# Optimization experiments

Hardware: AMD Instinct MI355X
Metric: run time of the kernel (lower is better)

Reference implementation:

```python
import jax, jax.numpy as jnp
import numpy as np

NUM_BINS = 10
HIST_RANGE = 10.0
LN_EPS = 1e-5
NUM_SERVERS = 64
START_IDX = 2 + 2 + NUM_SERVERS  # = 68


def layer_norm(x, g, b):
    mu = jnp.mean(x, axis=-1, keepdims=True)
    var = jnp.mean(jnp.square(x - mu), axis=-1, keepdims=True)
    return (x - mu) * jax.lax.rsqrt(var + LN_EPS) * g + b


def batched_histogram(w):
    # w: [B, S]; replicates np.histogram(w_i, bins=10, range=(0,10)) per row,
    # then normalizes by (sum + 1e-8). Values outside [0,10] are excluded;
    # value == 10 falls in the last bin.
    idx = jnp.clip(jnp.floor(w * (NUM_BINS / HIST_RANGE)).astype(jnp.int32), 0, NUM_BINS - 1)
    mask = ((w >= 0.0) & (w <= HIST_RANGE)).astype(w.dtype)
    oh = jax.nn.one_hot(idx, NUM_BINS, dtype=w.dtype) * mask[..., None]  # [B,S,NB]
    hist = jnp.sum(oh, axis=1)  # [B,NB]
    return hist / (jnp.sum(hist, axis=-1, keepdims=True) + 1e-8)


def setup_inputs() -> dict:
    key = jax.random.key(0)
    ks = jax.random.split(key, 16)
    B, OBS, ACT, H, NB = 65536, 512, 64, 128, NUM_BINS
    COMB = (OBS - NUM_SERVERS) + 128 + 64  # 640

    def lin(k, fin, fout):
        bound = 1.0 / np.sqrt(fin)
        kw, kb = jax.random.split(k)
        return (jax.random.uniform(kw, (fin, fout), jnp.float32, -bound, bound),
                jax.random.uniform(kb, (fout,), jnp.float32, -bound, bound))

    obs = jax.random.uniform(ks[0], (B, OBS), jnp.float32, 0.0, 10.0)
    preference = jax.random.uniform(ks[1], (B, 2), jnp.float32)
    h_w1, h_b1 = lin(ks[2], NB, H)
    h_w2, h_b2 = lin(ks[3], H, H)
    p_w, p_b = lin(ks[4], 2, 64)
    s_w1, s_b1 = lin(ks[5], COMB, 256)
    s_w2, s_b2 = lin(ks[6], 256, 256)
    qd_w, qd_b = lin(ks[7], 256, ACT)
    qe_w, qe_b = lin(ks[8], 256, ACT)
    return {
        'obs': obs, 'preference': preference,
        'h_w1': h_w1, 'h_b1': h_b1,
        'h_ln1_g': jnp.ones((H,)), 'h_ln1_b': jnp.zeros((H,)),
        'h_w2': h_w2, 'h_b2': h_b2,
        'h_ln2_g': jnp.ones((H,)), 'h_ln2_b': jnp.zeros((H,)),
        'p_w': p_w, 'p_b': p_b,
        'p_ln_g': jnp.ones((64,)), 'p_ln_b': jnp.zeros((64,)),
        's_w1': s_w1, 's_b1': s_b1,
        's_ln1_g': jnp.ones((256,)), 's_ln1_b': jnp.zeros((256,)),
        's_w2': s_w2, 's_b2': s_b2,
        's_ln2_g': jnp.ones((256,)), 's_ln2_b': jnp.zeros((256,)),
        'qd_w': qd_w, 'qd_b': qd_b, 'qe_w': qe_w, 'qe_b': qe_b,
    }


def reference(obs, preference,
              h_w1, h_b1, h_ln1_g, h_ln1_b, h_w2, h_b2, h_ln2_g, h_ln2_b,
              p_w, p_b, p_ln_g, p_ln_b,
              s_w1, s_b1, s_ln1_g, s_ln1_b, s_w2, s_b2, s_ln2_g, s_ln2_b,
              qd_w, qd_b, qe_w, qe_b):
    server_workloads = obs[:, START_IDX:START_IDX + NUM_SERVERS]
    obs_wo = jnp.concatenate([obs[:, :START_IDX], obs[:, START_IDX + NUM_SERVERS:]], axis=-1)

    hist = batched_histogram(server_workloads)  # [B, 10]
    h = layer_norm(jax.nn.relu(hist @ h_w1 + h_b1), h_ln1_g, h_ln1_b)
    h = layer_norm(jax.nn.relu(h @ h_w2 + h_b2), h_ln2_g, h_ln2_b)  # [B,128]

    p = layer_norm(jax.nn.relu(preference @ p_w + p_b), p_ln_g, p_ln_b)  # [B,64]

    combined = jnp.concatenate([obs_wo, h, p], axis=-1)  # [B,640]
    s = layer_norm(jax.nn.relu(combined @ s_w1 + s_b1), s_ln1_g, s_ln1_b)
    s = layer_norm(jax.nn.relu(s @ s_w2 + s_b2), s_ln2_g, s_ln2_b)  # [B,256]

    q_delay = s @ qd_w + qd_b   # [B,A]
    q_energy = s @ qe_w + qe_b  # [B,A]
    return jnp.stack([q_delay, q_energy], axis=-1)  # [B,A,2]
```

## Files before the change

### kernel.cpp

```cpp
#include <hip/hip_runtime.h>

typedef __bf16 bf16x8 __attribute__((ext_vector_type(8)));
typedef float  f32x4  __attribute__((ext_vector_type(4)));

#define OFF_W1  0
#define OFF_W2  163840
#define OFF_WQ  229376
#define OFF_WH1 262144
#define OFF_WH2 266240
#define WS_ELEMS 282624

__global__ __launch_bounds__(256) void prep_kernel(
    const float* __restrict__ s_w1, const float* __restrict__ s_w2,
    const float* __restrict__ qd_w, const float* __restrict__ qe_w,
    const float* __restrict__ h_w1, const float* __restrict__ h_w2,
    __bf16* __restrict__ wsb)
{
  int idx = blockIdx.x * 256 + threadIdx.x;
  if (idx >= WS_ELEMS) return;
  float val = 0.f;
  if (idx < OFF_W2) {
    int t = idx;
    int j = t & 7, l = (t >> 3) & 63, rest = t >> 9;
    int nt = rest & 15, ks = rest >> 4;
    int k = ks * 32 + (l >> 4) * 8 + j, n = nt * 16 + (l & 15);
    val = s_w1[k * 256 + n];
  } else if (idx < OFF_WQ) {
    int t = idx - OFF_W2;
    int j = t & 7, l = (t >> 3) & 63, rest = t >> 9;
    int nt = rest & 15, ks = rest >> 4;
    int k = ks * 32 + (l >> 4) * 8 + j, n = nt * 16 + (l & 15);
    val = s_w2[k * 256 + n];
  } else if (idx < OFF_WH1) {
    int t = idx - OFF_WQ;
    int j = t & 7, l = (t >> 3) & 63, rest = t >> 9;
    int nt = rest & 7, ks = rest >> 3;
    int k = ks * 32 + (l >> 4) * 8 + j, n = nt * 16 + (l & 15);
    int a = n >> 1;
    val = (n & 1) ? qe_w[k * 64 + a] : qd_w[k * 64 + a];
  } else if (idx < OFF_WH2) {
    int t = idx - OFF_WH1;
    int j = t & 7, l = (t >> 3) & 63, rest = t >> 9;
    int nt = rest & 7;
    int k = (l >> 4) * 8 + j, n = nt * 16 + (l & 15);
    val = (k < 10) ? h_w1[k * 128 + n] : 0.f;
  } else {
    int t = idx - OFF_WH2;
    int j = t & 7, l = (t >> 3) & 63, rest = t >> 9;
    int nt = rest & 7, ks = rest >> 3;
    int k = ks * 32 + (l >> 4) * 8 + j, n = nt * 16 + (l & 15);
    val = h_w2[k * 128 + n];
  }
  wsb[idx] = (__bf16)val;
}

template<int KSTEPS, int NT_TOT, int NTW>
__device__ __forceinline__ void run_gemm(const __bf16* A, int astride,
    const bf16x8* __restrict__ Bsw, int wave, int lane, f32x4 acc[2][NTW])
{
  const int quad = lane >> 4, ln = lane & 15;
  const int ntb = wave * NTW;
  bf16x8 bcur[NTW];
#pragma unroll
  for (int i = 0; i < NTW; ++i) bcur[i] = Bsw[(ntb + i) * 64 + lane];
#pragma unroll
  for (int ks = 0; ks < KSTEPS; ++ks) {
    bf16x8 bnxt[NTW];
    if (ks + 1 < KSTEPS) {
#pragma unroll
      for (int i = 0; i < NTW; ++i)
        bnxt[i] = Bsw[((ks + 1) * NT_TOT + ntb + i) * 64 + lane];
    }
    bf16x8 a[2];
#pragma unroll
    for (int mt = 0; mt < 2; ++mt)
      a[mt] = *(const bf16x8*)(A + (mt * 16 + ln) * astride + ks * 32 + quad * 8);
#pragma unroll
    for (int mt = 0; mt < 2; ++mt)
#pragma unroll
      for (int i = 0; i < NTW; ++i)
        acc[mt][i] = __builtin_amdgcn_mfma_f32_16x16x32_bf16(a[mt], bcur[i], acc[mt][i], 0, 0, 0);
    if (ks + 1 < KSTEPS) {
#pragma unroll
      for (int i = 0; i < NTW; ++i) bcur[i] = bnxt[i];
    }
  }
}

template<int W, int NTW>
__device__ __forceinline__ void epilogue_ln(f32x4 acc[2][NTW],
    const float* __restrict__ bias, const float* __restrict__ g, const float* __restrict__ bb,
    __bf16* Adst, int dstride, int dstcol0,
    float* red_s, float* red_q, int wave, int lane)
{
  const int quad = lane >> 4, ln = lane & 15;
  float x[2][NTW][4];
#pragma unroll
  for (int i = 0; i < NTW; ++i) {
    int n = (wave * NTW + i) * 16 + ln;
    float b = bias[n];
#pragma unroll
    for (int mt = 0; mt < 2; ++mt)
#pragma unroll
      for (int r = 0; r < 4; ++r)
        x[mt][i][r] = fmaxf(acc[mt][i][r] + b, 0.f);
  }
#pragma unroll
  for (int mt = 0; mt < 2; ++mt) {
    float s[4] = {0, 0, 0, 0}, q[4] = {0, 0, 0, 0};
#pragma unroll
    for (int i = 0; i < NTW; ++i)
#pragma unroll
      for (int r = 0; r < 4; ++r) { s[r] += x[mt][i][r]; q[r] += x[mt][i][r] * x[mt][i][r]; }
#pragma unroll
    for (int m2 = 1; m2 < 16; m2 <<= 1)
#pragma unroll
      for (int r = 0; r < 4; ++r) {
        s[r] += __shfl_xor(s[r], m2, 64);
        q[r] += __shfl_xor(q[r], m2, 64);
      }
    if (ln == 0) {
#pragma unroll
      for (int r = 0; r < 4; ++r) {
        int m = mt * 16 + quad * 4 + r;
        red_s[wave * 32 + m] = s[r];
        red_q[wave * 32 + m] = q[r];
      }
    }
  }
  __syncthreads();
#pragma unroll
  for (int mt = 0; mt < 2; ++mt)
#pragma unroll
    for (int r = 0; r < 4; ++r) {
      int m = mt * 16 + quad * 4 + r;
      float tot = 0.f, totq = 0.f;
#pragma unroll
      for (int w2 = 0; w2 < 8; ++w2) { tot += red_s[w2 * 32 + m]; totq += red_q[w2 * 32 + m]; }
      float mu = tot / (float)W;
      float var = totq / (float)W - mu * mu;
      float rs = rsqrtf(var + 1e-5f);
#pragma unroll
      for (int i = 0; i < NTW; ++i) {
        int n = (wave * NTW + i) * 16 + ln;
        float o = (x[mt][i][r] - mu) * rs * g[n] + bb[n];
        Adst[m * dstride + dstcol0 + n] = (__bf16)o;
      }
    }
  __syncthreads();
}

__global__ __launch_bounds__(512, 4) void critic_kernel(
    const float* __restrict__ obs, const float* __restrict__ pref,
    const float* __restrict__ h_b1, const float* __restrict__ h_g1, const float* __restrict__ h_bb1,
    const float* __restrict__ h_b2, const float* __restrict__ h_g2, const float* __restrict__ h_bb2,
    const float* __restrict__ p_w, const float* __restrict__ p_b,
    const float* __restrict__ p_g, const float* __restrict__ p_bb,
    const float* __restrict__ s_b1, const float* __restrict__ s_g1, const float* __restrict__ s_bb1,
    const float* __restrict__ s_b2, const float* __restrict__ s_g2, const float* __restrict__ s_bb2,
    const float* __restrict__ qd_b, const float* __restrict__ qe_b,
    const __bf16* __restrict__ wsb, float* __restrict__ out)
{
  __shared__ __align__(16) __bf16 A_comb[32 * 648];
  __shared__ __align__(16) __bf16 A_s[32 * 264];
  __shared__ __align__(16) __bf16 A_h[32 * 40];
  __shared__ float red_s[256];
  __shared__ float red_q[256];

  const int tid = threadIdx.x;
  const int wave = tid >> 6, lane = tid & 63;
  const int rowbase = blockIdx.x * 32;

  float pw0 = p_w[lane], pw1 = p_w[64 + lane], pb = p_b[lane];
  float pg = p_g[lane], pbb = p_bb[lane];
#pragma unroll
  for (int r = 0; r < 4; ++r) {
    int row = wave * 4 + r;
    int grow = rowbase + row;
    const float* orow = obs + (size_t)grow * 512;
#pragma unroll
    for (int j = 0; j < 7; ++j) {
      int col = lane + 64 * j;
      int src = (col < 68) ? col : col + 64;
      A_comb[row * 648 + col] = (__bf16)orow[src];
    }
    float w = orow[68 + lane];
    int bi = (int)floorf(w);
    bi = bi < 0 ? 0 : (bi > 9 ? 9 : bi);
    bool valid = (w >= 0.f) && (w <= 10.f);
    float tot = 0.f, mine = 0.f;
#pragma unroll
    for (int b = 0; b < 10; ++b) {
      unsigned long long mk = __ballot(valid && (bi == b));
      float c = (float)__popcll(mk);
      tot += c;
      if (lane == b) mine = c;
    }
    float inv = 1.f / (tot + 1e-8f);
    if (lane < 32) A_h[row * 40 + lane] = (__bf16)((lane < 10) ? mine * inv : 0.f);
    float a0 = pref[grow * 2], a1 = pref[grow * 2 + 1];
    float v = fmaxf(fmaf(a0, pw0, fmaf(a1, pw1, pb)), 0.f);
    float s1 = v, s2 = v * v;
#pragma unroll
    for (int m2 = 1; m2 < 64; m2 <<= 1) {
      s1 += __shfl_xor(s1, m2, 64);
      s2 += __shfl_xor(s2, m2, 64);
    }
    float mu = s1 * (1.f / 64.f);
    float var = s2 * (1.f / 64.f) - mu * mu;
    float o = (v - mu) * rsqrtf(var + 1e-5f) * pg + pbb;
    A_comb[row * 648 + 576 + lane] = (__bf16)o;
  }
  __syncthreads();

  {
    f32x4 acc[2][1] = {};
    run_gemm<1, 8, 1>(A_h, 40, (const bf16x8*)(wsb + OFF_WH1), wave, lane, acc);
    epilogue_ln<128, 1>(acc, h_b1, h_g1, h_bb1, A_s, 264, 0, red_s, red_q, wave, lane);
  }
  {
    f32x4 acc[2][1] = {};
    run_gemm<4, 8, 1>(A_s, 264, (const bf16x8*)(wsb + OFF_WH2), wave, lane, acc);
    epilogue_ln<128, 1>(acc, h_b2, h_g2, h_bb2, A_comb, 648, 448, red_s, red_q, wave, lane);
  }
  {
    f32x4 acc[2][2] = {};
    run_gemm<20, 16, 2>(A_comb, 648, (const bf16x8*)(wsb + OFF_W1), wave, lane, acc);
    epilogue_ln<256, 2>(acc, s_b1, s_g1, s_bb1, A_s, 264, 0, red_s, red_q, wave, lane);
  }
  {
    f32x4 acc[2][2] = {};
    run_gemm<8, 16, 2>(A_s, 264, (const bf16x8*)(wsb + OFF_W2), wave, lane, acc);
    epilogue_ln<256, 2>(acc, s_b2, s_g2, s_bb2, A_s, 264, 0, red_s, red_q, wave, lane);
  }
  {
    f32x4 acc[2][1] = {};
    run_gemm<8, 8, 1>(A_s, 264, (const bf16x8*)(wsb + OFF_WQ), wave, lane, acc);
    const int quad = lane >> 4, ln = lane & 15;
    int n = wave * 16 + ln;
    float qb = (n & 1) ? qe_b[n >> 1] : qd_b[n >> 1];
#pragma unroll
    for (int mt = 0; mt < 2; ++mt)
#pragma unroll
      for (int r = 0; r < 4; ++r) {
        int m = mt * 16 + quad * 4 + r;
        out[(size_t)(rowbase + m) * 128 + n] = acc[mt][0][r] + qb;
      }
  }
}

extern "C" void kernel_launch(void* const* d_in, const int* in_sizes, int n_in,
                              void* d_out, int out_size, void* d_ws, size_t ws_size,
                              hipStream_t stream) {
  const float* obs    = (const float*)d_in[0];
  const float* pref   = (const float*)d_in[1];
  const float* h_w1   = (const float*)d_in[2];
  const float* h_b1   = (const float*)d_in[3];
  const float* h_g1   = (const float*)d_in[4];
  const float* h_bb1  = (const float*)d_in[5];
  const float* h_w2   = (const float*)d_in[6];
  const float* h_b2   = (const float*)d_in[7];
  const float* h_g2   = (const float*)d_in[8];
  const float* h_bb2  = (const float*)d_in[9];
  const float* p_w    = (const float*)d_in[10];
  const float* p_b    = (const float*)d_in[11];
  const float* p_g    = (const float*)d_in[12];
  const float* p_bb   = (const float*)d_in[13];
  const float* s_w1   = (const float*)d_in[14];
  const float* s_b1   = (const float*)d_in[15];
  const float* s_g1   = (const float*)d_in[16];
  const float* s_bb1  = (const float*)d_in[17];
  const float* s_w2   = (const float*)d_in[18];
  const float* s_b2   = (const float*)d_in[19];
  const float* s_g2   = (const float*)d_in[20];
  const float* s_bb2  = (const float*)d_in[21];
  const float* qd_w   = (const float*)d_in[22];
  const float* qd_b   = (const float*)d_in[23];
  const float* qe_w   = (const float*)d_in[24];
  const float* qe_b   = (const float*)d_in[25];

  __bf16* wsb = (__bf16*)d_ws;
  int B = in_sizes[0] / 512;
  int nblocks = B / 32;

  prep_kernel<<<(WS_ELEMS + 255) / 256, 256, 0, stream>>>(s_w1, s_w2, qd_w, qe_w, h_w1, h_w2, wsb);
  critic_kernel<<<nblocks, 512, 0, stream>>>(
      obs, pref, h_b1, h_g1, h_bb1, h_b2, h_g2, h_bb2,
      p_w, p_b, p_g, p_bb, s_b1, s_g1, s_bb1, s_b2, s_g2, s_bb2,
      qd_b, qe_b, (const __bf16*)wsb, (float*)d_out);
}
```

Baseline: 377.5 us.

## Halve rows per block to 16, raise occupancy, vectorize obs loads

Each block now handles 16 batch rows instead of 32, so each wave issues one MFMA row tile per step. The launch bound rises to 8 blocks per CU and shared memory is cut, which raises occupancy and the block count. The obs gather now uses float4 loads with bf16x4 stores, and the layernorm reduction scratch is packed into float2. The cost is that each weight fragment loaded from global or L2 is reused across half as many rows, roughly doubling weight traffic per output row.

```diff
diff --git a/kernel.cpp b/kernel.cpp
--- a/kernel.cpp
+++ b/kernel.cpp
@@ -1,6 +1,7 @@
 #include <hip/hip_runtime.h>
 
 typedef __bf16 bf16x8 __attribute__((ext_vector_type(8)));
+typedef __bf16 bf16x4 __attribute__((ext_vector_type(4)));
 typedef float  f32x4  __attribute__((ext_vector_type(4)));
 
 #define OFF_W1  0
@@ -56,7 +57,7 @@
 
 template<int KSTEPS, int NT_TOT, int NTW>
 __device__ __forceinline__ void run_gemm(const __bf16* A, int astride,
-    const bf16x8* __restrict__ Bsw, int wave, int lane, f32x4 acc[2][NTW])
+    const bf16x8* __restrict__ Bsw, int wave, int lane, f32x4 acc[NTW])
 {
   const int quad = lane >> 4, ln = lane & 15;
   const int ntb = wave * NTW;
@@ -71,15 +72,10 @@
       for (int i = 0; i < NTW; ++i)
         bnxt[i] = Bsw[((ks + 1) * NT_TOT + ntb + i) * 64 + lane];
     }
-    bf16x8 a[2];
-#pragma unroll
-    for (int mt = 0; mt < 2; ++mt)
-      a[mt] = *(const bf16x8*)(A + (mt * 16 + ln) * astride + ks * 32 + quad * 8);
-#pragma unroll
-    for (int mt = 0; mt < 2; ++mt)
-#pragma unroll
-      for (int i = 0; i < NTW; ++i)
-        acc[mt][i] = __builtin_amdgcn_mfma_f32_16x16x32_bf16(a[mt], bcur[i], acc[mt][i], 0, 0, 0);
+    bf16x8 a = *(const bf16x8*)(A + ln * astride + ks * 32 + quad * 8);
+#pragma unroll
+    for (int i = 0; i < NTW; ++i)
+      acc[i] = __builtin_amdgcn_mfma_f32_16x16x32_bf16(a, bcur[i], acc[i], 0, 0, 0);
     if (ks + 1 < KSTEPS) {
 #pragma unroll
       for (int i = 0; i < NTW; ++i) bcur[i] = bnxt[i];
@@ -88,69 +84,62 @@
 }
 
 template<int W, int NTW>
-__device__ __forceinline__ void epilogue_ln(f32x4 acc[2][NTW],
+__device__ __forceinline__ void epilogue_ln(f32x4 acc[NTW],
     const float* __restrict__ bias, const float* __restrict__ g, const float* __restrict__ bb,
     __bf16* Adst, int dstride, int dstcol0,
-    float* red_s, float* red_q, int wave, int lane)
+    float2* red, int wave, int lane)
 {
   const int quad = lane >> 4, ln = lane & 15;
-  float x[2][NTW][4];
+  float x[NTW][4];
 #pragma unroll
   for (int i = 0; i < NTW; ++i) {
     int n = (wave * NTW + i) * 16 + ln;
     float b = bias[n];
 #pragma unroll
-    for (int mt = 0; mt < 2; ++mt)
-#pragma unroll
-      for (int r = 0; r < 4; ++r)
-        x[mt][i][r] = fmaxf(acc[mt][i][r] + b, 0.f);
-  }
-#pragma unroll
-  for (int mt = 0; mt < 2; ++mt) {
-    float s[4] = {0, 0, 0, 0}, q[4] = {0, 0, 0, 0};
-#pragma unroll
-    for (int i = 0; i < NTW; ++i)
-#pragma unroll
-      for (int r = 0; r < 4; ++r) { s[r] += x[mt][i][r]; q[r] += x[mt][i][r] * x[mt][i][r]; }
-#pragma unroll
-    for (int m2 = 1; m2 < 16; m2 <<= 1)
-#pragma unroll
-      for (int r = 0; r < 4; ++r) {
-        s[r] += __shfl_xor(s[r], m2, 64);
-        q[r] += __shfl_xor(q[r], m2, 64);
-      }
-    if (ln == 0) {
-#pragma unroll
-      for (int r = 0; r < 4; ++r) {
-        int m = mt * 16 + quad * 4 + r;
-        red_s[wave * 32 + m] = s[r];
-        red_q[wave * 32 + m] = q[r];
-      }
-    }
+    for (int r = 0; r < 4; ++r)
+      x[i][r] = fmaxf(acc[i][r] + b, 0.f);
+  }
+  float s[4] = {0, 0, 0, 0}, q[4] = {0, 0, 0, 0};
+#pragma unroll
+  for (int i = 0; i < NTW; ++i)
+#pragma unroll
+    for (int r = 0; r < 4; ++r) { s[r] += x[i][r]; q[r] += x[i][r] * x[i][r]; }
+#pragma unroll
+  for (int m2 = 1; m2 < 16; m2 <<= 1)
+#pragma unroll
+    for (int r = 0; r < 4; ++r) {
+      s[r] += __shfl_xor(s[r], m2, 64);
+      q[r] += __shfl_xor(q[r], m2, 64);
+    }
+  if (ln == 0) {
+#pragma unroll
+    for (int r = 0; r < 4; ++r)
+      red[wave * 16 + quad * 4 + r] = make_float2(s[r], q[r]);
   }
   __syncthreads();
 #pragma unroll
-  for (int mt = 0; mt < 2; ++mt)
-#pragma unroll
-    for (int r = 0; r < 4; ++r) {
-      int m = mt * 16 + quad * 4 + r;
-      float tot = 0.f, totq = 0.f;
-#pragma unroll
-      for (int w2 = 0; w2 < 8; ++w2) { tot += red_s[w2 * 32 + m]; totq += red_q[w2 * 32 + m]; }
-      float mu = tot / (float)W;
-      float var = totq / (float)W - mu * mu;
-      float rs = rsqrtf(var + 1e-5f);
-#pragma unroll
-      for (int i = 0; i < NTW; ++i) {
-        int n = (wave * NTW + i) * 16 + ln;
-        float o = (x[mt][i][r] - mu) * rs * g[n] + bb[n];
-        Adst[m * dstride + dstcol0 + n] = (__bf16)o;
-      }
-    }
+  for (int r = 0; r < 4; ++r) {
+    int m = quad * 4 + r;
+    float tot = 0.f, totq = 0.f;
+#pragma unroll
+    for (int w2 = 0; w2 < 8; ++w2) {
+      float2 t = red[w2 * 16 + m];
+      tot += t.x; totq += t.y;
+    }
+    float mu = tot / (float)W;
+    float var = totq / (float)W - mu * mu;
+    float rs = rsqrtf(var + 1e-5f);
+#pragma unroll
+    for (int i = 0; i < NTW; ++i) {
+      int n = (wave * NTW + i) * 16 + ln;
+      float o = (x[i][r] - mu) * rs * g[n] + bb[n];
+      Adst[m * dstride + dstcol0 + n] = (__bf16)o;
+    }
+  }
   __syncthreads();
 }
 
-__global__ __launch_bounds__(512, 4) void critic_kernel(
+__global__ __launch_bounds__(512, 8) void critic_kernel(
     const float* __restrict__ obs, const float* __restrict__ pref,
     const float* __restrict__ h_b1, const float* __restrict__ h_g1, const float* __restrict__ h_bb1,
     const float* __restrict__ h_b2, const float* __restrict__ h_g2, const float* __restrict__ h_bb2,
@@ -161,28 +150,32 @@
     const float* __restrict__ qd_b, const float* __restrict__ qe_b,
     const __bf16* __restrict__ wsb, float* __restrict__ out)
 {
-  __shared__ __align__(16) __bf16 A_comb[32 * 648];
-  __shared__ __align__(16) __bf16 A_s[32 * 264];
-  __shared__ __align__(16) __bf16 A_h[32 * 40];
-  __shared__ float red_s[256];
-  __shared__ float red_q[256];
+  __shared__ __align__(16) __bf16 A_comb[16 * 648];
+  __shared__ __align__(16) __bf16 A_s[16 * 264];
+  __shared__ __align__(16) __bf16 A_h[16 * 40];
+  __shared__ float2 red[128];
 
   const int tid = threadIdx.x;
   const int wave = tid >> 6, lane = tid & 63;
-  const int rowbase = blockIdx.x * 32;
+  const int rowbase = blockIdx.x * 16;
 
   float pw0 = p_w[lane], pw1 = p_w[64 + lane], pb = p_b[lane];
   float pg = p_g[lane], pbb = p_bb[lane];
 #pragma unroll
-  for (int r = 0; r < 4; ++r) {
-    int row = wave * 4 + r;
+  for (int r = 0; r < 2; ++r) {
+    int row = wave * 2 + r;
     int grow = rowbase + row;
     const float* orow = obs + (size_t)grow * 512;
 #pragma unroll
-    for (int j = 0; j < 7; ++j) {
-      int col = lane + 64 * j;
-      int src = (col < 68) ? col : col + 64;
-      A_comb[row * 648 + col] = (__bf16)orow[src];
+    for (int j = 0; j < 2; ++j) {
+      int l = lane + 64 * j;
+      if (l < 112) {
+        int src4 = (l < 17) ? l : l + 16;
+        float4 v = *(const float4*)(orow + 4 * src4);
+        bf16x4 o;
+        o[0] = (__bf16)v.x; o[1] = (__bf16)v.y; o[2] = (__bf16)v.z; o[3] = (__bf16)v.w;
+        *(bf16x4*)(&A_comb[row * 648 + 4 * l]) = o;
+      }
     }
     float w = orow[68 + lane];
     int bi = (int)floorf(w);
@@ -214,38 +207,36 @@
   __syncthreads();
 
   {
-    f32x4 acc[2][1] = {};
+    f32x4 acc[1] = {};
     run_gemm<1, 8, 1>(A_h, 40, (const bf16x8*)(wsb + OFF_WH1), wave, lane, acc);
-    epilogue_ln<128, 1>(acc, h_b1, h_g1, h_bb1, A_s, 264, 0, red_s, red_q, wave, lane);
-  }
-  {
-    f32x4 acc[2][1] = {};
+    epilogue_ln<128, 1>(acc, h_b1, h_g1, h_bb1, A_s, 264, 0, red, wave, lane);
+  }
+  {
+    f32x4 acc[1] = {};
     run_gemm<4, 8, 1>(A_s, 264, (const bf16x8*)(wsb + OFF_WH2), wave, lane, acc);
-    epilogue_ln<128, 1>(acc, h_b2, h_g2, h_bb2, A_comb, 648, 448, red_s, red_q, wave, lane);
-  }
-  {
-    f32x4 acc[2][2] = {};
+    epilogue_ln<128, 1>(acc, h_b2, h_g2, h_bb2, A_comb, 648, 448, red, wave, lane);
+  }
+  {
+    f32x4 acc[2] = {};
     run_gemm<20, 16, 2>(A_comb, 648, (const bf16x8*)(wsb + OFF_W1), wave, lane, acc);
-    epilogue_ln<256, 2>(acc, s_b1, s_g1, s_bb1, A_s, 264, 0, red_s, red_q, wave, lane);
-  }
-  {
-    f32x4 acc[2][2] = {};
+    epilogue_ln<256, 2>(acc, s_b1, s_g1, s_bb1, A_s, 264, 0, red, wave, lane);
+  }
+  {
+    f32x4 acc[2] = {};
     run_gemm<8, 16, 2>(A_s, 264, (const bf16x8*)(wsb + OFF_W2), wave, lane, acc);
-    epilogue_ln<256, 2>(acc, s_b2, s_g2, s_bb2, A_s, 264, 0, red_s, red_q, wave, lane);
-  }
-  {
-    f32x4 acc[2][1] = {};
+    epilogue_ln<256, 2>(acc, s_b2, s_g2, s_bb2, A_s, 264, 0, red, wave, lane);
+  }
+  {
+    f32x4 acc[1] = {};
     run_gemm<8, 8, 1>(A_s, 264, (const bf16x8*)(wsb + OFF_WQ), wave, lane, acc);
     const int quad = lane >> 4, ln = lane & 15;
     int n = wave * 16 + ln;
     float qb = (n & 1) ? qe_b[n >> 1] : qd_b[n >> 1];
 #pragma unroll
-    for (int mt = 0; mt < 2; ++mt)
-#pragma unroll
-      for (int r = 0; r < 4; ++r) {
-        int m = mt * 16 + quad * 4 + r;
-        out[(size_t)(rowbase + m) * 128 + n] = acc[mt][0][r] + qb;
-      }
+    for (int r = 0; r < 4; ++r) {
+      int m = quad * 4 + r;
+      out[(size_t)(rowbase + m) * 128 + n] = acc[0][r] + qb;
+    }
   }
 }
 
@@ -281,7 +272,7 @@
 
   __bf16* wsb = (__bf16*)d_ws;
   int B = in_sizes[0] / 512;
-  int nblocks = B / 32;
+  int nblocks = B / 16;
 
   prep_kernel<<<(WS_ELEMS + 255) / 256, 256, 0, stream>>>(s_w1, s_w2, qd_w, qe_w, h_w1, h_w2, wsb);
   critic_kernel<<<nblocks, 512, 0, stream>>>(
```

After: 368.9 us. -2.3%, faster.

## Stream obs A-fragments from global into MFMA, shrink LDS, raise occupancy

Applied to the files above, without the earlier changes.

Stops staging the 448 non-server obs columns in a large LDS buffer. The first big GEMM now loads those A fragments straight from global memory as float4 and converts them to bf16 in registers, using a special offset for the k-step that skips the server columns. Only the hist and pref features stay in a small LDS buffer. This cuts LDS use per block, and launch bounds are raised to 8 blocks per CU. The LN reduction is also packed into float2. The trade-off is uncoalesced, strided global reads inside the MFMA loop with exposed latency, in place of a coalesced prefetch.

```diff
diff --git a/kernel.cpp b/kernel.cpp
--- a/kernel.cpp
+++ b/kernel.cpp
@@ -1,6 +1,7 @@
 #include <hip/hip_runtime.h>
 
 typedef __bf16 bf16x8 __attribute__((ext_vector_type(8)));
+typedef __bf16 bf16x4 __attribute__((ext_vector_type(4)));
 typedef float  f32x4  __attribute__((ext_vector_type(4)));
 
 #define OFF_W1  0
@@ -55,31 +56,29 @@
 }
 
 template<int KSTEPS, int NT_TOT, int NTW>
-__device__ __forceinline__ void run_gemm(const __bf16* A, int astride,
-    const bf16x8* __restrict__ Bsw, int wave, int lane, f32x4 acc[2][NTW])
+__device__ __forceinline__ void run_gemm2(const __bf16* A, int astride,
+    const bf16x8* __restrict__ Bsw, int nt0, int lane, f32x4 acc[2][NTW])
 {
   const int quad = lane >> 4, ln = lane & 15;
-  const int ntb = wave * NTW;
+  const __bf16* ar = A + ln * astride + quad * 8;
   bf16x8 bcur[NTW];
 #pragma unroll
-  for (int i = 0; i < NTW; ++i) bcur[i] = Bsw[(ntb + i) * 64 + lane];
+  for (int i = 0; i < NTW; ++i) bcur[i] = Bsw[(nt0 + i) * 64 + lane];
 #pragma unroll
   for (int ks = 0; ks < KSTEPS; ++ks) {
     bf16x8 bnxt[NTW];
     if (ks + 1 < KSTEPS) {
 #pragma unroll
       for (int i = 0; i < NTW; ++i)
-        bnxt[i] = Bsw[((ks + 1) * NT_TOT + ntb + i) * 64 + lane];
-    }
-    bf16x8 a[2];
-#pragma unroll
-    for (int mt = 0; mt < 2; ++mt)
-      a[mt] = *(const bf16x8*)(A + (mt * 16 + ln) * astride + ks * 32 + quad * 8);
-#pragma unroll
-    for (int mt = 0; mt < 2; ++mt)
-#pragma unroll
-      for (int i = 0; i < NTW; ++i)
-        acc[mt][i] = __builtin_amdgcn_mfma_f32_16x16x32_bf16(a[mt], bcur[i], acc[mt][i], 0, 0, 0);
+        bnxt[i] = Bsw[((ks + 1) * NT_TOT + nt0 + i) * 64 + lane];
+    }
+    bf16x8 a0 = *(const bf16x8*)(ar + ks * 32);
+    bf16x8 a1 = *(const bf16x8*)(ar + 16 * astride + ks * 32);
+#pragma unroll
+    for (int i = 0; i < NTW; ++i) {
+      acc[0][i] = __builtin_amdgcn_mfma_f32_16x16x32_bf16(a0, bcur[i], acc[0][i], 0, 0, 0);
+      acc[1][i] = __builtin_amdgcn_mfma_f32_16x16x32_bf16(a1, bcur[i], acc[1][i], 0, 0, 0);
+    }
     if (ks + 1 < KSTEPS) {
 #pragma unroll
       for (int i = 0; i < NTW; ++i) bcur[i] = bnxt[i];
@@ -88,16 +87,16 @@
 }
 
 template<int W, int NTW>
-__device__ __forceinline__ void epilogue_ln(f32x4 acc[2][NTW],
+__device__ __forceinline__ void epilogue_ln2(f32x4 acc[2][NTW],
     const float* __restrict__ bias, const float* __restrict__ g, const float* __restrict__ bb,
-    __bf16* Adst, int dstride, int dstcol0,
-    float* red_s, float* red_q, int wave, int lane)
+    int nt0, __bf16* Adst, int dstride, int dstcol0,
+    float2* red, int wave, int lane)
 {
   const int quad = lane >> 4, ln = lane & 15;
   float x[2][NTW][4];
 #pragma unroll
   for (int i = 0; i < NTW; ++i) {
-    int n = (wave * NTW + i) * 16 + ln;
+    int n = (nt0 + i) * 16 + ln;
     float b = bias[n];
 #pragma unroll
     for (int mt = 0; mt < 2; ++mt)
@@ -121,11 +120,8 @@
       }
     if (ln == 0) {
 #pragma unroll
-      for (int r = 0; r < 4; ++r) {
-        int m = mt * 16 + quad * 4 + r;
-        red_s[wave * 32 + m] = s[r];
-        red_q[wave * 32 + m] = q[r];
-      }
+      for (int r = 0; r < 4; ++r)
+        red[wave * 32 + mt * 16 + quad * 4 + r] = make_float2(s[r], q[r]);
     }
   }
   __syncthreads();
@@ -136,13 +132,16 @@
       int m = mt * 16 + quad * 4 + r;
       float tot = 0.f, totq = 0.f;
 #pragma unroll
-      for (int w2 = 0; w2 < 8; ++w2) { tot += red_s[w2 * 32 + m]; totq += red_q[w2 * 32 + m]; }
+      for (int w2 = 0; w2 < 8; ++w2) {
+        float2 t = red[w2 * 32 + m];
+        tot += t.x; totq += t.y;
+      }
       float mu = tot / (float)W;
       float var = totq / (float)W - mu * mu;
       float rs = rsqrtf(var + 1e-5f);
 #pragma unroll
       for (int i = 0; i < NTW; ++i) {
-        int n = (wave * NTW + i) * 16 + ln;
+        int n = (nt0 + i) * 16 + ln;
         float o = (x[mt][i][r] - mu) * rs * g[n] + bb[n];
         Adst[m * dstride + dstcol0 + n] = (__bf16)o;
       }
@@ -150,7 +149,7 @@
   __syncthreads();
 }
 
-__global__ __launch_bounds__(512, 4) void critic_kernel(
+__global__ __launch_bounds__(512, 8) void critic_kernel(
     const float* __restrict__ obs, const float* __restrict__ pref,
     const float* __restrict__ h_b1, const float* __restrict__ h_g1, const float* __restrict__ h_bb1,
     const float* __restrict__ h_b2, const float* __restrict__ h_g2, const float* __restrict__ h_bb2,
@@ -161,14 +160,14 @@
     const float* __restrict__ qd_b, const float* __restrict__ qe_b,
     const __bf16* __restrict__ wsb, float* __restrict__ out)
 {
-  __shared__ __align__(16) __bf16 A_comb[32 * 648];
   __shared__ __align__(16) __bf16 A_s[32 * 264];
+  __shared__ __align__(16) __bf16 A2[32 * 200];
   __shared__ __align__(16) __bf16 A_h[32 * 40];
-  __shared__ float red_s[256];
-  __shared__ float red_q[256];
+  __shared__ __align__(16) float2 red[8 * 32];
 
   const int tid = threadIdx.x;
   const int wave = tid >> 6, lane = tid & 63;
+  const int ln = lane & 15, quad = lane >> 4;
   const int rowbase = blockIdx.x * 32;
 
   float pw0 = p_w[lane], pw1 = p_w[64 + lane], pb = p_b[lane];
@@ -178,12 +177,6 @@
     int row = wave * 4 + r;
     int grow = rowbase + row;
     const float* orow = obs + (size_t)grow * 512;
-#pragma unroll
-    for (int j = 0; j < 7; ++j) {
-      int col = lane + 64 * j;
-      int src = (col < 68) ? col : col + 64;
-      A_comb[row * 648 + col] = (__bf16)orow[src];
-    }
     float w = orow[68 + lane];
     int bi = (int)floorf(w);
     bi = bi < 0 ? 0 : (bi > 9 ? 9 : bi);
@@ -200,43 +193,80 @@
     if (lane < 32) A_h[row * 40 + lane] = (__bf16)((lane < 10) ? mine * inv : 0.f);
     float a0 = pref[grow * 2], a1 = pref[grow * 2 + 1];
     float v = fmaxf(fmaf(a0, pw0, fmaf(a1, pw1, pb)), 0.f);
-    float s1 = v, s2 = v * v;
+    float s1v = v, s2v = v * v;
 #pragma unroll
     for (int m2 = 1; m2 < 64; m2 <<= 1) {
-      s1 += __shfl_xor(s1, m2, 64);
-      s2 += __shfl_xor(s2, m2, 64);
-    }
-    float mu = s1 * (1.f / 64.f);
-    float var = s2 * (1.f / 64.f) - mu * mu;
+      s1v += __shfl_xor(s1v, m2, 64);
+      s2v += __shfl_xor(s2v, m2, 64);
+    }
+    float mu = s1v * (1.f / 64.f);
+    float var = s2v * (1.f / 64.f) - mu * mu;
     float o = (v - mu) * rsqrtf(var + 1e-5f) * pg + pbb;
-    A_comb[row * 648 + 576 + lane] = (__bf16)o;
+    A2[row * 200 + 128 + lane] = (__bf16)o;
   }
   __syncthreads();
 
   {
     f32x4 acc[2][1] = {};
-    run_gemm<1, 8, 1>(A_h, 40, (const bf16x8*)(wsb + OFF_WH1), wave, lane, acc);
-    epilogue_ln<128, 1>(acc, h_b1, h_g1, h_bb1, A_s, 264, 0, red_s, red_q, wave, lane);
+    run_gemm2<1, 8, 1>(A_h, 40, (const bf16x8*)(wsb + OFF_WH1), wave, lane, acc);
+    epilogue_ln2<128, 1>(acc, h_b1, h_g1, h_bb1, wave, A_s, 264, 0, red, wave, lane);
   }
   {
     f32x4 acc[2][1] = {};
-    run_gemm<4, 8, 1>(A_s, 264, (const bf16x8*)(wsb + OFF_WH2), wave, lane, acc);
-    epilogue_ln<128, 1>(acc, h_b2, h_g2, h_bb2, A_comb, 648, 448, red_s, red_q, wave, lane);
+    run_gemm2<4, 8, 1>(A_s, 264, (const bf16x8*)(wsb + OFF_WH2), wave, lane, acc);
+    epilogue_ln2<128, 1>(acc, h_b2, h_g2, h_bb2, wave, A2, 200, 0, red, wave, lane);
   }
   {
     f32x4 acc[2][2] = {};
-    run_gemm<20, 16, 2>(A_comb, 648, (const bf16x8*)(wsb + OFF_W1), wave, lane, acc);
-    epilogue_ln<256, 2>(acc, s_b1, s_g1, s_bb1, A_s, 264, 0, red_s, red_q, wave, lane);
+    const bf16x8* B1 = (const bf16x8*)(wsb + OFF_W1);
+    const int nt0 = wave * 2;
+    bf16x8 bcur[2];
+    bcur[0] = B1[nt0 * 64 + lane];
+    bcur[1] = B1[(nt0 + 1) * 64 + lane];
+    const float* ga0 = obs + (size_t)(rowbase + ln) * 512 + quad * 8;
+    const float* ga1 = ga0 + 16 * 512;
+    const __bf16* la = A2 + ln * 200 + quad * 8;
+#pragma unroll
+    for (int ks = 0; ks < 20; ++ks) {
+      bf16x8 bnxt[2];
+      if (ks + 1 < 20) {
+        bnxt[0] = B1[((ks + 1) * 16 + nt0) * 64 + lane];
+        bnxt[1] = B1[((ks + 1) * 16 + nt0 + 1) * 64 + lane];
+      }
+      bf16x8 a0, a1;
+      if (ks < 14) {
+        int o1, o2;
+        if (ks < 2)        { o1 = ks * 32;              o2 = o1 + 4; }
+        else if (ks == 2)  { o1 = (quad == 0) ? 64 : 128; o2 = 132; }
+        else               { o1 = ks * 32 + 64;         o2 = o1 + 4; }
+        float4 v00 = *(const float4*)(ga0 + o1);
+        float4 v01 = *(const float4*)(ga0 + o2);
+        float4 v10 = *(const float4*)(ga1 + o1);
+        float4 v11 = *(const float4*)(ga1 + o2);
+        a0[0] = (__bf16)v00.x; a0[1] = (__bf16)v00.y; a0[2] = (__bf16)v00.z; a0[3] = (__bf16)v00.w;
+        a0[4] = (__bf16)v01.x; a0[5] = (__bf16)v01.y; a0[6] = (__bf16)v01.z; a0[7] = (__bf16)v01.w;
+        a1[0] = (__bf16)v10.x; a1[1] = (__bf16)v10.y; a1[2] = (__bf16)v10.z; a1[3] = (__bf16)v10.w;
+        a1[4] = (__bf16)v11.x; a1[5] = (__bf16)v11.y; a1[6] = (__bf16)v11.z; a1[7] = (__bf16)v11.w;
+      } else {
+        a0 = *(const bf16x8*)(la + (ks - 14) * 32);
+        a1 = *(const bf16x8*)(la + 16 * 200 + (ks - 14) * 32);
+      }
+      acc[0][0] = __builtin_amdgcn_mfma_f32_16x16x32_bf16(a0, bcur[0], acc[0][0], 0, 0, 0);
+      acc[1][0] = __builtin_amdgcn_mfma_f32_16x16x32_bf16(a1, bcur[0], acc[1][0], 0, 0, 0);
+      acc[0][1] = __builtin_amdgcn_mfma_f32_16x16x32_bf16(a0, bcur[1], acc[0][1], 0, 0, 0);
+      acc[1][1] = __builtin_amdgcn_mfma_f32_16x16x32_bf16(a1, bcur[1], acc[1][1], 0, 0, 0);
+      if (ks + 1 < 20) { bcur[0] = bnxt[0]; bcur[1] = bnxt[1]; }
+    }
+    epilogue_ln2<256, 2>(acc, s_b1, s_g1, s_bb1, nt0, A_s, 264, 0, red, wave, lane);
   }
   {
     f32x4 acc[2][2] = {};
-    run_gemm<8, 16, 2>(A_s, 264, (const bf16x8*)(wsb + OFF_W2), wave, lane, acc);
-    epilogue_ln<256, 2>(acc, s_b2, s_g2, s_bb2, A_s, 264, 0, red_s, red_q, wave, lane);
+    run_gemm2<8, 16, 2>(A_s, 264, (const bf16x8*)(wsb + OFF_W2), wave * 2, lane, acc);
+    epilogue_ln2<256, 2>(acc, s_b2, s_g2, s_bb2, wave * 2, A_s, 264, 0, red, wave, lane);
   }
   {
     f32x4 acc[2][1] = {};
-    run_gemm<8, 8, 1>(A_s, 264, (const bf16x8*)(wsb + OFF_WQ), wave, lane, acc);
-    const int quad = lane >> 4, ln = lane & 15;
+    run_gemm2<8, 8, 1>(A_s, 264, (const bf16x8*)(wsb + OFF_WQ), wave, lane, acc);
     int n = wave * 16 + ln;
     float qb = (n & 1) ? qe_b[n >> 1] : qd_b[n >> 1];
 #pragma unroll
```

New measurement: 396.1 us. +4.9%, slower.
